# Kernel tuning notes

Hardware: AMD Instinct MI355X
Metric: run time of the kernel (lower is better)

Reference implementation:

```python
import jax, jax.numpy as jnp
import numpy as np

N_NODES = 50000
N_EDGES = 400000


def _gcn_norm(edge_index, num_nodes):
    """Add self-loops and compute symmetric GCN normalization coefficients.

    Returns (src, dst, norm) where out[dst] += norm * h[src].
    """
    loop = jnp.arange(num_nodes, dtype=edge_index.dtype)
    src = jnp.concatenate([edge_index[0], loop])
    dst = jnp.concatenate([edge_index[1], loop])
    ones = jnp.ones(src.shape[0], dtype=jnp.float32)
    deg = jax.ops.segment_sum(ones, dst, num_segments=num_nodes)
    d_inv_sqrt = jnp.where(deg > 0, jax.lax.rsqrt(jnp.maximum(deg, 1.0)), 0.0)
    norm = d_inv_sqrt[src] * d_inv_sqrt[dst]
    return src, dst, norm


def _gcn_conv(x, W, b, src, dst, norm, num_nodes):
    h = x @ W                              # [N, out] dense GEMM first (PyG GCNConv order)
    msg = h[src] * norm[:, None]           # [E+N, out] gather + scale
    agg = jax.ops.segment_sum(msg, dst, num_segments=num_nodes)  # scatter-add
    return agg + b


def setup_inputs() -> dict:
    key = jax.random.key(0)
    k1, k2, k3, k4, k5, k6 = jax.random.split(key, 6)
    x = jax.random.normal(k1, (N_NODES, 128), dtype=jnp.float32)
    edge_index = jax.random.randint(k2, (2, N_EDGES), 0, N_NODES, dtype=jnp.int64)
    # Glorot-ish scaled params
    W1 = jax.random.normal(k3, (128, 512), dtype=jnp.float32) * (1.0 / np.sqrt(128))
    b1 = jnp.zeros((512,), dtype=jnp.float32)
    W2 = jax.random.normal(k4, (512, 250), dtype=jnp.float32) * (1.0 / np.sqrt(512))
    b2 = jnp.zeros((250,), dtype=jnp.float32)
    return {"x": x, "edge_index": edge_index, "W1": W1, "b1": b1, "W2": W2, "b2": b2}


def reference(x, edge_index, W1, b1, W2, b2):
    num_nodes = x.shape[0]
    src, dst, norm = _gcn_norm(edge_index, num_nodes)
    h = _gcn_conv(x, W1, b1, src, dst, norm, num_nodes)
    h = jax.nn.relu(h)
    h = _gcn_conv(h, W2, b2, src, dst, norm, num_nodes)
    return jax.nn.relu(h)
```

## Files before the change

### kernel.cpp

```cpp
#include <hip/hip_runtime.h>

constexpr int NN  = 50000;
constexpr int NE  = 400000;
constexpr int F0  = 128;
constexpr int F1  = 512;
constexpr int F2  = 250;
constexpr int MT64 = 782;
constexpr int SLOT = 64;

typedef short  short8 __attribute__((ext_vector_type(8)));
typedef float  f32x4  __attribute__((ext_vector_type(4)));

__device__ inline unsigned short f2bf(float f) {
    union { float f; unsigned u; } v; v.f = f;
    unsigned u = v.u;
    return (unsigned short)((u + 0x7FFFu + ((u >> 16) & 1u)) >> 16);
}
__device__ inline float bf2f(unsigned short h) {
    union { unsigned u; float f; } v; v.u = ((unsigned)h) << 16;
    return v.f;
}
__device__ inline float bflo(unsigned u) {
    union { unsigned u; float f; } v; v.u = u << 16; return v.f;
}
__device__ inline float bfhi(unsigned u) {
    union { unsigned u; float f; } v; v.u = u & 0xFFFF0000u; return v.f;
}

__global__ void k_build(const int4* __restrict__ src4, const int4* __restrict__ dst4,
                        int* __restrict__ cnt, int* __restrict__ slot) {
    int t = blockIdx.x * 256 + threadIdx.x;
    if (t >= NE / 4) return;
    int4 s = src4[t];
    int4 d = dst4[t];
    int p;
    p = atomicAdd(&cnt[d.x], 1); if (p < SLOT) slot[d.x * SLOT + p] = s.x;
    p = atomicAdd(&cnt[d.y], 1); if (p < SLOT) slot[d.y * SLOT + p] = s.y;
    p = atomicAdd(&cnt[d.z], 1); if (p < SLOT) slot[d.z * SLOT + p] = s.z;
    p = atomicAdd(&cnt[d.w], 1); if (p < SLOT) slot[d.w * SLOT + p] = s.w;
}

__global__ __launch_bounds__(256) void k_prep(
        const float4* __restrict__ x4, const int* __restrict__ cnt,
        ushort4* __restrict__ xs,
        const float* __restrict__ W1, unsigned short* __restrict__ w1t,
        const float* __restrict__ W2, unsigned short* __restrict__ w2t) {
    int b = blockIdx.x;
    if (b < 6250) {
        int t = b * 256 + threadIdx.x;
        float dn = rsqrtf((float)cnt[t >> 5] + 1.0f);
        float4 v = x4[t];
        ushort4 o;
        o.x = f2bf(dn * v.x); o.y = f2bf(dn * v.y);
        o.z = f2bf(dn * v.z); o.w = f2bf(dn * v.w);
        xs[t] = o;
    } else if (b < 6250 + 256) {
        int t = (b - 6250) * 256 + threadIdx.x;
        int n = t >> 7, k = t & 127;
        w1t[t] = f2bf(W1[k * F1 + n]);
    } else {
        int t = (b - 6506) * 256 + threadIdx.x;
        int n = t >> 9, k = t & 511;
        w2t[t] = (n < F2) ? f2bf(W2[k * F2 + n]) : (unsigned short)0;
    }
}

__global__ __launch_bounds__(256) void k_gather1(
        const unsigned int* __restrict__ xs, const int* __restrict__ slot,
        const int* __restrict__ cnt, unsigned int* __restrict__ agg) {
    int n = blockIdx.x * 4 + (threadIdx.x >> 6);
    int c = threadIdx.x & 63;
    if (n >= NN) return;
    int deg = cnt[n]; if (deg > SLOT) deg = SLOT;
    float dn = rsqrtf((float)deg + 1.0f);
    const int* sl = slot + n * SLOT;
    unsigned a = xs[(size_t)n * 64 + c];
    float s0 = bflo(a), s1 = bfhi(a);
    int j = 0;
    for (; j + 8 <= deg; j += 8) {
        int i0 = sl[j],     i1 = sl[j + 1], i2 = sl[j + 2], i3 = sl[j + 3];
        int i4 = sl[j + 4], i5 = sl[j + 5], i6 = sl[j + 6], i7 = sl[j + 7];
        unsigned v0 = xs[(size_t)i0 * 64 + c];
        unsigned v1 = xs[(size_t)i1 * 64 + c];
        unsigned v2 = xs[(size_t)i2 * 64 + c];
        unsigned v3 = xs[(size_t)i3 * 64 + c];
        unsigned v4 = xs[(size_t)i4 * 64 + c];
        unsigned v5 = xs[(size_t)i5 * 64 + c];
        unsigned v6 = xs[(size_t)i6 * 64 + c];
        unsigned v7 = xs[(size_t)i7 * 64 + c];
        s0 += bflo(v0) + bflo(v1) + bflo(v2) + bflo(v3)
            + bflo(v4) + bflo(v5) + bflo(v6) + bflo(v7);
        s1 += bfhi(v0) + bfhi(v1) + bfhi(v2) + bfhi(v3)
            + bfhi(v4) + bfhi(v5) + bfhi(v6) + bfhi(v7);
    }
    for (; j + 4 <= deg; j += 4) {
        int i0 = sl[j], i1 = sl[j + 1], i2 = sl[j + 2], i3 = sl[j + 3];
        unsigned v0 = xs[(size_t)i0 * 64 + c];
        unsigned v1 = xs[(size_t)i1 * 64 + c];
        unsigned v2 = xs[(size_t)i2 * 64 + c];
        unsigned v3 = xs[(size_t)i3 * 64 + c];
        s0 += bflo(v0) + bflo(v1) + bflo(v2) + bflo(v3);
        s1 += bfhi(v0) + bfhi(v1) + bfhi(v2) + bfhi(v3);
    }
    for (; j < deg; ++j) {
        unsigned v = xs[(size_t)sl[j] * 64 + c];
        s0 += bflo(v); s1 += bfhi(v);
    }
    agg[(size_t)n * 64 + c] =
        (unsigned)f2bf(dn * s0) | ((unsigned)f2bf(dn * s1) << 16);
}

__global__ __launch_bounds__(256) void k_gemm1(
        const unsigned short* __restrict__ A,
        const unsigned short* __restrict__ Bt,
        unsigned short* __restrict__ C,
        const float* __restrict__ bias, int M)
{
    __shared__ unsigned short As[64 * 128];
    __shared__ unsigned short Bs[128 * 128];

    const int tid = threadIdx.x;
    const int wv = tid >> 6, ln = tid & 63;
    const int m0 = blockIdx.y * 64, n0 = blockIdx.x * 128;
    const int wy = wv >> 1, wx = wv & 1;
    const int lane15 = ln & 15, quad = ln >> 4;

#pragma unroll
    for (int i = 0; i < 4; ++i) {
        int c = i * 256 + tid;
        int m = c >> 4, q = c & 15;
        int gq = q ^ (m & 15);
        int arow = m0 + m; if (arow > M - 1) arow = M - 1;
        __builtin_amdgcn_global_load_lds(
            (const __attribute__((address_space(1))) void*)(A + (size_t)arow * 128 + gq * 8),
            (__attribute__((address_space(3))) void*)(As + (i * 4 + wv) * 512), 16, 0, 0);
    }
#pragma unroll
    for (int i = 0; i < 8; ++i) {
        int c = i * 256 + tid;
        int n = c >> 4, q = c & 15;
        int gq = q ^ (n & 15);
        __builtin_amdgcn_global_load_lds(
            (const __attribute__((address_space(1))) void*)(Bt + (size_t)(n0 + n) * 128 + gq * 8),
            (__attribute__((address_space(3))) void*)(Bs + (i * 4 + wv) * 512), 16, 0, 0);
    }

    f32x4 acc[2][4];
#pragma unroll
    for (int fy = 0; fy < 2; ++fy)
#pragma unroll
        for (int fx = 0; fx < 4; ++fx)
            acc[fy][fx] = (f32x4)0.0f;

    __syncthreads();

#pragma unroll
    for (int kk = 0; kk < 4; ++kk) {
        short8 af[2], bf[4];
#pragma unroll
        for (int f = 0; f < 2; ++f) {
            int mA = wy * 32 + f * 16 + lane15;
            int sA = (kk * 4 + quad) ^ (mA & 15);
            af[f] = *(const short8*)(As + mA * 128 + sA * 8);
        }
#pragma unroll
        for (int f = 0; f < 4; ++f) {
            int nB = wx * 64 + f * 16 + lane15;
            int sB = (kk * 4 + quad) ^ (nB & 15);
            bf[f] = *(const short8*)(Bs + nB * 128 + sB * 8);
        }
#pragma unroll
        for (int fy = 0; fy < 2; ++fy)
#pragma unroll
            for (int fx = 0; fx < 4; ++fx)
                acc[fy][fx] = __builtin_amdgcn_mfma_f32_16x16x32_bf16(
                    af[fy], bf[fx], acc[fy][fx], 0, 0, 0);
    }

#pragma unroll
    for (int fy = 0; fy < 2; ++fy) {
        int rowb = m0 + wy * 32 + fy * 16 + quad * 4;
#pragma unroll
        for (int fx = 0; fx < 4; ++fx) {
            int col = n0 + wx * 64 + fx * 16 + lane15;
            float bia = bias[col];
            f32x4 v = acc[fy][fx];
#pragma unroll
            for (int r = 0; r < 4; ++r) {
                int row = rowb + r;
                if (row < M)
                    C[(size_t)row * F1 + col] = f2bf(fmaxf(v[r] + bia, 0.0f));
            }
        }
    }
}

__global__ __launch_bounds__(256) void k_gemm2(
        const unsigned short* __restrict__ A,
        const unsigned short* __restrict__ Bt,
        unsigned short* __restrict__ C,
        const int* __restrict__ cnt, int M)
{
    __shared__ unsigned short As[2][64 * 32];
    __shared__ unsigned short Bs[2][256 * 32];

    const int tid = threadIdx.x;
    const int wv = tid >> 6, ln = tid & 63;
    const int m0 = blockIdx.x * 64;
    const int wy = wv >> 1, wx = wv & 1;
    const int lane15 = ln & 15, quad = ln >> 4;

    const int mA_ = tid >> 2, qA = tid & 3;
    const int gqA = qA ^ ((mA_ >> 1) & 3);
    int arow = m0 + mA_; if (arow > M - 1) arow = M - 1;
    const unsigned short* agp = A + (size_t)arow * F1 + gqA * 8;
    const int aofs = wv * 512;

    const unsigned short* bgp[4];
    int bofs[4];
#pragma unroll
    for (int i = 0; i < 4; ++i) {
        int c = (i * 4 + wv) * 64 + ln;
        int n = c >> 2, q = c & 3;
        int gq = q ^ ((n >> 1) & 3);
        bgp[i] = Bt + (size_t)n * F1 + gq * 8;
        bofs[i] = (i * 4 + wv) * 512;
    }

    f32x4 acc[2][8];
#pragma unroll
    for (int fy = 0; fy < 2; ++fy)
#pragma unroll
        for (int fx = 0; fx < 8; ++fx)
            acc[fy][fx] = (f32x4)0.0f;

    const int NK = F1 / 32;

    __builtin_amdgcn_global_load_lds(
        (const __attribute__((address_space(1))) void*)agp,
        (__attribute__((address_space(3))) void*)(&As[0][0] + aofs), 16, 0, 0);
#pragma unroll
    for (int i = 0; i < 4; ++i)
        __builtin_amdgcn_global_load_lds(
            (const __attribute__((address_space(1))) void*)bgp[i],
            (__attribute__((address_space(3))) void*)(&Bs[0][0] + bofs[i]), 16, 0, 0);

    for (int ks = 0; ks < NK; ++ks) {
        __syncthreads();
        if (ks + 1 < NK) {
            int ko = (ks + 1) << 5;
            int nb = (ks + 1) & 1;
            __builtin_amdgcn_global_load_lds(
                (const __attribute__((address_space(1))) void*)(agp + ko),
                (__attribute__((address_space(3))) void*)(&As[nb][0] + aofs), 16, 0, 0);
#pragma unroll
            for (int i = 0; i < 4; ++i)
                __builtin_amdgcn_global_load_lds(
                    (const __attribute__((address_space(1))) void*)(bgp[i] + ko),
                    (__attribute__((address_space(3))) void*)(&Bs[nb][0] + bofs[i]), 16, 0, 0);
        }
        const int b = ks & 1;
        short8 af[2], bf[8];
#pragma unroll
        for (int f = 0; f < 2; ++f) {
            int mA = wy * 32 + f * 16 + lane15;
            int sA = quad ^ ((mA >> 1) & 3);
            af[f] = *(const short8*)(&As[b][0] + mA * 32 + sA * 8);
        }
#pragma unroll
        for (int f = 0; f < 8; ++f) {
            int nB = wx * 128 + f * 16 + lane15;
            int sB = quad ^ ((nB >> 1) & 3);
            bf[f] = *(const short8*)(&Bs[b][0] + nB * 32 + sB * 8);
        }
#pragma unroll
        for (int fy = 0; fy < 2; ++fy)
#pragma unroll
            for (int fx = 0; fx < 8; ++fx)
                acc[fy][fx] = __builtin_amdgcn_mfma_f32_16x16x32_bf16(
                    af[fy], bf[fx], acc[fy][fx], 0, 0, 0);
    }

#pragma unroll
    for (int fy = 0; fy < 2; ++fy) {
        int rowb = m0 + wy * 32 + fy * 16 + quad * 4;
        float rs[4];
#pragma unroll
        for (int r = 0; r < 4; ++r) {
            int row = rowb + r; if (row > M - 1) row = M - 1;
            rs[r] = rsqrtf((float)cnt[row] + 1.0f);
        }
#pragma unroll
        for (int fx = 0; fx < 8; ++fx) {
            int col = wx * 128 + fx * 16 + lane15;
            f32x4 v = acc[fy][fx];
#pragma unroll
            for (int r = 0; r < 4; ++r) {
                int row = rowb + r;
                if (row < M)
                    C[(size_t)row * 256 + col] = f2bf(v[r] * rs[r]);
            }
        }
    }
}

__global__ __launch_bounds__(256) void k_gather2(
        const ushort4* __restrict__ t4, const int* __restrict__ slot,
        const int* __restrict__ cnt, const float* __restrict__ b2,
        float* __restrict__ out) {
    int n = blockIdx.x * 4 + (threadIdx.x >> 6);
    int c = threadIdx.x & 63;
    if (n >= NN) return;
    int deg = cnt[n]; if (deg > SLOT) deg = SLOT;
    float dn = rsqrtf((float)deg + 1.0f);
    const int* sl = slot + n * SLOT;
    ushort4 a = t4[(size_t)n * 64 + c];
    float sx = bf2f(a.x), sy = bf2f(a.y), sz = bf2f(a.z), sw = bf2f(a.w);
    int j = 0;
    for (; j + 8 <= deg; j += 8) {
        int i0 = sl[j],     i1 = sl[j + 1], i2 = sl[j + 2], i3 = sl[j + 3];
        int i4 = sl[j + 4], i5 = sl[j + 5], i6 = sl[j + 6], i7 = sl[j + 7];
        ushort4 v0 = t4[(size_t)i0 * 64 + c];
        ushort4 v1 = t4[(size_t)i1 * 64 + c];
        ushort4 v2 = t4[(size_t)i2 * 64 + c];
        ushort4 v3 = t4[(size_t)i3 * 64 + c];
        ushort4 v4 = t4[(size_t)i4 * 64 + c];
        ushort4 v5 = t4[(size_t)i5 * 64 + c];
        ushort4 v6 = t4[(size_t)i6 * 64 + c];
        ushort4 v7 = t4[(size_t)i7 * 64 + c];
        sx += bf2f(v0.x) + bf2f(v1.x) + bf2f(v2.x) + bf2f(v3.x)
            + bf2f(v4.x) + bf2f(v5.x) + bf2f(v6.x) + bf2f(v7.x);
        sy += bf2f(v0.y) + bf2f(v1.y) + bf2f(v2.y) + bf2f(v3.y)
            + bf2f(v4.y) + bf2f(v5.y) + bf2f(v6.y) + bf2f(v7.y);
        sz += bf2f(v0.z) + bf2f(v1.z) + bf2f(v2.z) + bf2f(v3.z)
            + bf2f(v4.z) + bf2f(v5.z) + bf2f(v6.z) + bf2f(v7.z);
        sw += bf2f(v0.w) + bf2f(v1.w) + bf2f(v2.w) + bf2f(v3.w)
            + bf2f(v4.w) + bf2f(v5.w) + bf2f(v6.w) + bf2f(v7.w);
    }
    for (; j + 4 <= deg; j += 4) {
        int i0 = sl[j], i1 = sl[j + 1], i2 = sl[j + 2], i3 = sl[j + 3];
        ushort4 v0 = t4[(size_t)i0 * 64 + c];
        ushort4 v1 = t4[(size_t)i1 * 64 + c];
        ushort4 v2 = t4[(size_t)i2 * 64 + c];
        ushort4 v3 = t4[(size_t)i3 * 64 + c];
        sx += bf2f(v0.x) + bf2f(v1.x) + bf2f(v2.x) + bf2f(v3.x);
        sy += bf2f(v0.y) + bf2f(v1.y) + bf2f(v2.y) + bf2f(v3.y);
        sz += bf2f(v0.z) + bf2f(v1.z) + bf2f(v2.z) + bf2f(v3.z);
        sw += bf2f(v0.w) + bf2f(v1.w) + bf2f(v2.w) + bf2f(v3.w);
    }
    for (; j < deg; ++j) {
        ushort4 v = t4[(size_t)sl[j] * 64 + c];
        sx += bf2f(v.x); sy += bf2f(v.y); sz += bf2f(v.z); sw += bf2f(v.w);
    }
    int f = c * 4;
    float* o = out + (size_t)n * F2;
    if (f     < F2) o[f]     = fmaxf(dn * sx + b2[f],     0.f);
    if (f + 1 < F2) o[f + 1] = fmaxf(dn * sy + b2[f + 1], 0.f);
    if (f + 2 < F2) o[f + 2] = fmaxf(dn * sz + b2[f + 2], 0.f);
    if (f + 3 < F2) o[f + 3] = fmaxf(dn * sw + b2[f + 3], 0.f);
}

extern "C" void kernel_launch(void* const* d_in, const int* in_sizes, int n_in,
                              void* d_out, int out_size, void* d_ws, size_t ws_size,
                              hipStream_t stream) {
    const float* x  = (const float*)d_in[0];
    const int*   ei = (const int*)d_in[1];
    const float* W1 = (const float*)d_in[2];
    const float* b1 = (const float*)d_in[3];
    const float* W2 = (const float*)d_in[4];
    const float* b2 = (const float*)d_in[5];
    float* out = (float*)d_out;

    char* p = (char*)d_ws;
    auto carve = [&](size_t bytes) { char* r = p; p += (bytes + 255) & ~(size_t)255; return r; };
    int*            cnt  = (int*)carve(NN * 4);
    int*            slot = (int*)carve((size_t)NN * SLOT * 4);
    unsigned short* xs   = (unsigned short*)carve((size_t)NN * F0 * 2);
    unsigned short* agg1 = (unsigned short*)carve((size_t)NN * F0 * 2);
    unsigned short* h1   = (unsigned short*)carve((size_t)NN * F1 * 2);
    unsigned short* t2s  = (unsigned short*)carve((size_t)NN * 256 * 2);
    unsigned short* w1t  = (unsigned short*)carve((size_t)F1 * F0 * 2);
    unsigned short* w2t  = (unsigned short*)carve((size_t)256 * F1 * 2);

    hipMemsetAsync(cnt, 0, NN * sizeof(int), stream);
    k_build<<<(NE / 4 + 255) / 256, 256, 0, stream>>>(
        (const int4*)ei, (const int4*)(ei + NE), cnt, slot);
    k_prep<<<6250 + 256 + 512, 256, 0, stream>>>(
        (const float4*)x, cnt, (ushort4*)xs, W1, w1t, W2, w2t);
    k_gather1<<<(NN + 3) / 4, 256, 0, stream>>>((const unsigned int*)xs, slot, cnt,
                                                (unsigned int*)agg1);
    k_gemm1<<<dim3(F1 / 128, MT64), 256, 0, stream>>>(agg1, w1t, h1, b1, NN);
    k_gemm2<<<MT64, 256, 0, stream>>>(h1, w2t, t2s, cnt, NN);
    k_gather2<<<(NN + 3) / 4, 256, 0, stream>>>((const ushort4*)t2s, slot, cnt, b2, out);
}
```

Baseline: 238.7 us.

## Merge graph build with prep, move source-degree scaling into gather, enlarge GEMM2 tile

The CSR-slot build and the input/weight conversion now run in one launch. Because the conversion no longer depends on degree counts, the per-source normalization moves into the first gather, which reads cnt[src] and applies an rsqrt per neighbor. GEMM2 now uses 128-row tiles with 4x8 accumulators per wave to improve reuse of the B operand. The 4-wide remainder loops in both gathers are removed. The cost is extra cnt loads and rsqrt in gather1, higher register pressure in GEMM2, and fewer GEMM2 blocks (391).

```diff
diff --git a/kernel.cpp b/kernel.cpp
--- a/kernel.cpp
+++ b/kernel.cpp
@@ -6,6 +6,7 @@
 constexpr int F1  = 512;
 constexpr int F2  = 250;
 constexpr int MT64 = 782;
+constexpr int MT128 = 391;
 constexpr int SLOT = 64;
 
 typedef short  short8 __attribute__((ext_vector_type(8)));
@@ -27,39 +28,39 @@
     union { unsigned u; float f; } v; v.u = u & 0xFFFF0000u; return v.f;
 }
 
-__global__ void k_build(const int4* __restrict__ src4, const int4* __restrict__ dst4,
-                        int* __restrict__ cnt, int* __restrict__ slot) {
-    int t = blockIdx.x * 256 + threadIdx.x;
-    if (t >= NE / 4) return;
-    int4 s = src4[t];
-    int4 d = dst4[t];
-    int p;
-    p = atomicAdd(&cnt[d.x], 1); if (p < SLOT) slot[d.x * SLOT + p] = s.x;
-    p = atomicAdd(&cnt[d.y], 1); if (p < SLOT) slot[d.y * SLOT + p] = s.y;
-    p = atomicAdd(&cnt[d.z], 1); if (p < SLOT) slot[d.z * SLOT + p] = s.z;
-    p = atomicAdd(&cnt[d.w], 1); if (p < SLOT) slot[d.w * SLOT + p] = s.w;
-}
-
-__global__ __launch_bounds__(256) void k_prep(
-        const float4* __restrict__ x4, const int* __restrict__ cnt,
-        ushort4* __restrict__ xs,
+#define GLDS(src, dst) __builtin_amdgcn_global_load_lds( \
+    (const __attribute__((address_space(1))) void*)(src), \
+    (__attribute__((address_space(3))) void*)(dst), 16, 0, 0)
+
+__global__ __launch_bounds__(256) void k_setup(
+        const int4* __restrict__ src4, const int4* __restrict__ dst4,
+        int* __restrict__ cnt, int* __restrict__ slot,
+        const float4* __restrict__ x4, ushort4* __restrict__ xs,
         const float* __restrict__ W1, unsigned short* __restrict__ w1t,
         const float* __restrict__ W2, unsigned short* __restrict__ w2t) {
     int b = blockIdx.x;
-    if (b < 6250) {
+    if (b < 391) {
         int t = b * 256 + threadIdx.x;
-        float dn = rsqrtf((float)cnt[t >> 5] + 1.0f);
+        if (t >= NE / 4) return;
+        int4 s = src4[t];
+        int4 d = dst4[t];
+        int p;
+        p = atomicAdd(&cnt[d.x], 1); if (p < SLOT) slot[d.x * SLOT + p] = s.x;
+        p = atomicAdd(&cnt[d.y], 1); if (p < SLOT) slot[d.y * SLOT + p] = s.y;
+        p = atomicAdd(&cnt[d.z], 1); if (p < SLOT) slot[d.z * SLOT + p] = s.z;
+        p = atomicAdd(&cnt[d.w], 1); if (p < SLOT) slot[d.w * SLOT + p] = s.w;
+    } else if (b < 391 + 6250) {
+        int t = (b - 391) * 256 + threadIdx.x;
         float4 v = x4[t];
         ushort4 o;
-        o.x = f2bf(dn * v.x); o.y = f2bf(dn * v.y);
-        o.z = f2bf(dn * v.z); o.w = f2bf(dn * v.w);
+        o.x = f2bf(v.x); o.y = f2bf(v.y); o.z = f2bf(v.z); o.w = f2bf(v.w);
         xs[t] = o;
-    } else if (b < 6250 + 256) {
-        int t = (b - 6250) * 256 + threadIdx.x;
+    } else if (b < 391 + 6250 + 256) {
+        int t = (b - 6641) * 256 + threadIdx.x;
         int n = t >> 7, k = t & 127;
         w1t[t] = f2bf(W1[k * F1 + n]);
     } else {
-        int t = (b - 6506) * 256 + threadIdx.x;
+        int t = (b - 6897) * 256 + threadIdx.x;
         int n = t >> 9, k = t & 511;
         w2t[t] = (n < F2) ? f2bf(W2[k * F2 + n]) : (unsigned short)0;
     }
@@ -71,15 +72,24 @@
     int n = blockIdx.x * 4 + (threadIdx.x >> 6);
     int c = threadIdx.x & 63;
     if (n >= NN) return;
-    int deg = cnt[n]; if (deg > SLOT) deg = SLOT;
+    int deg = cnt[n];
     float dn = rsqrtf((float)deg + 1.0f);
+    if (deg > SLOT) deg = SLOT;
     const int* sl = slot + n * SLOT;
     unsigned a = xs[(size_t)n * 64 + c];
-    float s0 = bflo(a), s1 = bfhi(a);
+    float s0 = dn * bflo(a), s1 = dn * bfhi(a);
     int j = 0;
     for (; j + 8 <= deg; j += 8) {
         int i0 = sl[j],     i1 = sl[j + 1], i2 = sl[j + 2], i3 = sl[j + 3];
         int i4 = sl[j + 4], i5 = sl[j + 5], i6 = sl[j + 6], i7 = sl[j + 7];
+        float w0 = rsqrtf((float)cnt[i0] + 1.0f);
+        float w1 = rsqrtf((float)cnt[i1] + 1.0f);
+        float w2 = rsqrtf((float)cnt[i2] + 1.0f);
+        float w3 = rsqrtf((float)cnt[i3] + 1.0f);
+        float w4 = rsqrtf((float)cnt[i4] + 1.0f);
+        float w5 = rsqrtf((float)cnt[i5] + 1.0f);
+        float w6 = rsqrtf((float)cnt[i6] + 1.0f);
+        float w7 = rsqrtf((float)cnt[i7] + 1.0f);
         unsigned v0 = xs[(size_t)i0 * 64 + c];
         unsigned v1 = xs[(size_t)i1 * 64 + c];
         unsigned v2 = xs[(size_t)i2 * 64 + c];
@@ -88,23 +98,16 @@
         unsigned v5 = xs[(size_t)i5 * 64 + c];
         unsigned v6 = xs[(size_t)i6 * 64 + c];
         unsigned v7 = xs[(size_t)i7 * 64 + c];
-        s0 += bflo(v0) + bflo(v1) + bflo(v2) + bflo(v3)
-            + bflo(v4) + bflo(v5) + bflo(v6) + bflo(v7);
-        s1 += bfhi(v0) + bfhi(v1) + bfhi(v2) + bfhi(v3)
-            + bfhi(v4) + bfhi(v5) + bfhi(v6) + bfhi(v7);
-    }
-    for (; j + 4 <= deg; j += 4) {
-        int i0 = sl[j], i1 = sl[j + 1], i2 = sl[j + 2], i3 = sl[j + 3];
-        unsigned v0 = xs[(size_t)i0 * 64 + c];
-        unsigned v1 = xs[(size_t)i1 * 64 + c];
-        unsigned v2 = xs[(size_t)i2 * 64 + c];
-        unsigned v3 = xs[(size_t)i3 * 64 + c];
-        s0 += bflo(v0) + bflo(v1) + bflo(v2) + bflo(v3);
-        s1 += bfhi(v0) + bfhi(v1) + bfhi(v2) + bfhi(v3);
+        s0 += w0 * bflo(v0) + w1 * bflo(v1) + w2 * bflo(v2) + w3 * bflo(v3)
+            + w4 * bflo(v4) + w5 * bflo(v5) + w6 * bflo(v6) + w7 * bflo(v7);
+        s1 += w0 * bfhi(v0) + w1 * bfhi(v1) + w2 * bfhi(v2) + w3 * bfhi(v3)
+            + w4 * bfhi(v4) + w5 * bfhi(v5) + w6 * bfhi(v6) + w7 * bfhi(v7);
     }
     for (; j < deg; ++j) {
-        unsigned v = xs[(size_t)sl[j] * 64 + c];
-        s0 += bflo(v); s1 += bfhi(v);
+        int s = sl[j];
+        float w = rsqrtf((float)cnt[s] + 1.0f);
+        unsigned v = xs[(size_t)s * 64 + c];
+        s0 += w * bflo(v); s1 += w * bfhi(v);
     }
     agg[(size_t)n * 64 + c] =
         (unsigned)f2bf(dn * s0) | ((unsigned)f2bf(dn * s1) << 16);
@@ -131,18 +134,14 @@
         int m = c >> 4, q = c & 15;
         int gq = q ^ (m & 15);
         int arow = m0 + m; if (arow > M - 1) arow = M - 1;
-        __builtin_amdgcn_global_load_lds(
-            (const __attribute__((address_space(1))) void*)(A + (size_t)arow * 128 + gq * 8),
-            (__attribute__((address_space(3))) void*)(As + (i * 4 + wv) * 512), 16, 0, 0);
+        GLDS(A + (size_t)arow * 128 + gq * 8, As + (i * 4 + wv) * 512);
     }
 #pragma unroll
     for (int i = 0; i < 8; ++i) {
         int c = i * 256 + tid;
         int n = c >> 4, q = c & 15;
         int gq = q ^ (n & 15);
-        __builtin_amdgcn_global_load_lds(
-            (const __attribute__((address_space(1))) void*)(Bt + (size_t)(n0 + n) * 128 + gq * 8),
-            (__attribute__((address_space(3))) void*)(Bs + (i * 4 + wv) * 512), 16, 0, 0);
+        GLDS(Bt + (size_t)(n0 + n) * 128 + gq * 8, Bs + (i * 4 + wv) * 512);
     }
 
     f32x4 acc[2][4];
@@ -201,21 +200,26 @@
         unsigned short* __restrict__ C,
         const int* __restrict__ cnt, int M)
 {
-    __shared__ unsigned short As[2][64 * 32];
+    __shared__ unsigned short As[2][128 * 32];
     __shared__ unsigned short Bs[2][256 * 32];
 
     const int tid = threadIdx.x;
     const int wv = tid >> 6, ln = tid & 63;
-    const int m0 = blockIdx.x * 64;
-    const int wy = wv >> 1, wx = wv & 1;
+    const int m0 = blockIdx.x * 128;
+    const int wy = wv & 1, wx = wv >> 1;
     const int lane15 = ln & 15, quad = ln >> 4;
 
-    const int mA_ = tid >> 2, qA = tid & 3;
-    const int gqA = qA ^ ((mA_ >> 1) & 3);
-    int arow = m0 + mA_; if (arow > M - 1) arow = M - 1;
-    const unsigned short* agp = A + (size_t)arow * F1 + gqA * 8;
-    const int aofs = wv * 512;
-
+    const unsigned short* agp[2];
+    int aofs[2];
+#pragma unroll
+    for (int i = 0; i < 2; ++i) {
+        int c = (i * 4 + wv) * 64 + ln;
+        int m = c >> 2, q = c & 3;
+        int gq = q ^ ((m >> 1) & 3);
+        int ar = m0 + m; if (ar > M - 1) ar = M - 1;
+        agp[i] = A + (size_t)ar * F1 + gq * 8;
+        aofs[i] = (i * 4 + wv) * 512;
+    }
     const unsigned short* bgp[4];
     int bofs[4];
 #pragma unroll
@@ -227,43 +231,39 @@
         bofs[i] = (i * 4 + wv) * 512;
     }
 
-    f32x4 acc[2][8];
-#pragma unroll
-    for (int fy = 0; fy < 2; ++fy)
+    f32x4 acc[4][8];
+#pragma unroll
+    for (int fy = 0; fy < 4; ++fy)
 #pragma unroll
         for (int fx = 0; fx < 8; ++fx)
             acc[fy][fx] = (f32x4)0.0f;
 
     const int NK = F1 / 32;
 
-    __builtin_amdgcn_global_load_lds(
-        (const __attribute__((address_space(1))) void*)agp,
-        (__attribute__((address_space(3))) void*)(&As[0][0] + aofs), 16, 0, 0);
+#pragma unroll
+    for (int i = 0; i < 2; ++i)
+        GLDS(agp[i], &As[0][0] + aofs[i]);
 #pragma unroll
     for (int i = 0; i < 4; ++i)
-        __builtin_amdgcn_global_load_lds(
-            (const __attribute__((address_space(1))) void*)bgp[i],
-            (__attribute__((address_space(3))) void*)(&Bs[0][0] + bofs[i]), 16, 0, 0);
+        GLDS(bgp[i], &Bs[0][0] + bofs[i]);
 
     for (int ks = 0; ks < NK; ++ks) {
         __syncthreads();
         if (ks + 1 < NK) {
             int ko = (ks + 1) << 5;
             int nb = (ks + 1) & 1;
-            __builtin_amdgcn_global_load_lds(
-                (const __attribute__((address_space(1))) void*)(agp + ko),
-                (__attribute__((address_space(3))) void*)(&As[nb][0] + aofs), 16, 0, 0);
+#pragma unroll
+            for (int i = 0; i < 2; ++i)
+                GLDS(agp[i] + ko, &As[nb][0] + aofs[i]);
 #pragma unroll
             for (int i = 0; i < 4; ++i)
-                __builtin_amdgcn_global_load_lds(
-                    (const __attribute__((address_space(1))) void*)(bgp[i] + ko),
-                    (__attribute__((address_space(3))) void*)(&Bs[nb][0] + bofs[i]), 16, 0, 0);
+                GLDS(bgp[i] + ko, &Bs[nb][0] + bofs[i]);
         }
         const int b = ks & 1;
-        short8 af[2], bf[8];
-#pragma unroll
-        for (int f = 0; f < 2; ++f) {
-            int mA = wy * 32 + f * 16 + lane15;
+        short8 af[4], bf[8];
+#pragma unroll
+        for (int f = 0; f < 4; ++f) {
+            int mA = wy * 64 + f * 16 + lane15;
             int sA = quad ^ ((mA >> 1) & 3);
             af[f] = *(const short8*)(&As[b][0] + mA * 32 + sA * 8);
         }
@@ -274,7 +274,7 @@
             bf[f] = *(const short8*)(&Bs[b][0] + nB * 32 + sB * 8);
         }
 #pragma unroll
-        for (int fy = 0; fy < 2; ++fy)
+        for (int fy = 0; fy < 4; ++fy)
 #pragma unroll
             for (int fx = 0; fx < 8; ++fx)
                 acc[fy][fx] = __builtin_amdgcn_mfma_f32_16x16x32_bf16(
@@ -282,8 +282,8 @@
     }
 
 #pragma unroll
-    for (int fy = 0; fy < 2; ++fy) {
-        int rowb = m0 + wy * 32 + fy * 16 + quad * 4;
+    for (int fy = 0; fy < 4; ++fy) {
+        int rowb = m0 + wy * 64 + fy * 16 + quad * 4;
         float rs[4];
 #pragma unroll
         for (int r = 0; r < 4; ++r) {
@@ -311,8 +311,9 @@
     int n = blockIdx.x * 4 + (threadIdx.x >> 6);
     int c = threadIdx.x & 63;
     if (n >= NN) return;
-    int deg = cnt[n]; if (deg > SLOT) deg = SLOT;
+    int deg = cnt[n];
     float dn = rsqrtf((float)deg + 1.0f);
+    if (deg > SLOT) deg = SLOT;
     const int* sl = slot + n * SLOT;
     ushort4 a = t4[(size_t)n * 64 + c];
     float sx = bf2f(a.x), sy = bf2f(a.y), sz = bf2f(a.z), sw = bf2f(a.w);
@@ -337,17 +338,6 @@
         sw += bf2f(v0.w) + bf2f(v1.w) + bf2f(v2.w) + bf2f(v3.w)
             + bf2f(v4.w) + bf2f(v5.w) + bf2f(v6.w) + bf2f(v7.w);
     }
-    for (; j + 4 <= deg; j += 4) {
-        int i0 = sl[j], i1 = sl[j + 1], i2 = sl[j + 2], i3 = sl[j + 3];
-        ushort4 v0 = t4[(size_t)i0 * 64 + c];
-        ushort4 v1 = t4[(size_t)i1 * 64 + c];
-        ushort4 v2 = t4[(size_t)i2 * 64 + c];
-        ushort4 v3 = t4[(size_t)i3 * 64 + c];
-        sx += bf2f(v0.x) + bf2f(v1.x) + bf2f(v2.x) + bf2f(v3.x);
-        sy += bf2f(v0.y) + bf2f(v1.y) + bf2f(v2.y) + bf2f(v3.y);
-        sz += bf2f(v0.z) + bf2f(v1.z) + bf2f(v2.z) + bf2f(v3.z);
-        sw += bf2f(v0.w) + bf2f(v1.w) + bf2f(v2.w) + bf2f(v3.w);
-    }
     for (; j < deg; ++j) {
         ushort4 v = t4[(size_t)sl[j] * 64 + c];
         sx += bf2f(v.x); sy += bf2f(v.y); sz += bf2f(v.z); sw += bf2f(v.w);
@@ -383,13 +373,12 @@
     unsigned short* w2t  = (unsigned short*)carve((size_t)256 * F1 * 2);
 
     hipMemsetAsync(cnt, 0, NN * sizeof(int), stream);
-    k_build<<<(NE / 4 + 255) / 256, 256, 0, stream>>>(
-        (const int4*)ei, (const int4*)(ei + NE), cnt, slot);
-    k_prep<<<6250 + 256 + 512, 256, 0, stream>>>(
-        (const float4*)x, cnt, (ushort4*)xs, W1, w1t, W2, w2t);
+    k_setup<<<391 + 6250 + 256 + 512, 256, 0, stream>>>(
+        (const int4*)ei, (const int4*)(ei + NE), cnt, slot,
+        (const float4*)x, (ushort4*)xs, W1, w1t, W2, w2t);
     k_gather1<<<(NN + 3) / 4, 256, 0, stream>>>((const unsigned int*)xs, slot, cnt,
                                                 (unsigned int*)agg1);
     k_gemm1<<<dim3(F1 / 128, MT64), 256, 0, stream>>>(agg1, w1t, h1, b1, NN);
-    k_gemm2<<<MT64, 256, 0, stream>>>(h1, w2t, t2s, cnt, NN);
+    k_gemm2<<<MT128, 256, 0, stream>>>(h1, w2t, t2s, cnt, NN);
     k_gather2<<<(NN + 3) / 4, 256, 0, stream>>>((const ushort4*)t2s, slot, cnt, b2, out);
 }
```

Result: slower. 267.5 us (+12.1%).
